# Performance work log

Measured on AMD Instinct MI355X. Metric: run time of the kernel, lower is better.

Reference implementation:

```python
import math
import jax, jax.numpy as jnp
import numpy as np

B, N = 1, 512
C_S, C_Z, H, C, P_Q, P_V = 384, 128, 12, 16, 4, 8
CAT = C_Z * H + C * H + 3 * H * P_V + 1  # 2017


def _apply(t_r, t_t, x):
    # t_r: (b,n,3,3), t_t: (b,n,3), x: (b,3,h,p,n) -> global frame coords
    xg = jnp.einsum('bnij,bjhpn->bihpn', t_r, x)
    return xg + jnp.swapaxes(t_t, 1, 2)[:, :, None, None, :]


def setup_inputs() -> dict:
    key = jax.random.key(0)
    ks = jax.random.split(key, 14)
    f = lambda k, shp: jax.random.normal(k, shp, dtype=jnp.float32)
    return {
        's': f(ks[0], (B, C_S, N)),
        'z': f(ks[1], (B, C_Z, N, N)),
        't_r': f(ks[2], (B, N, 3, 3)),
        't_t': f(ks[3], (B, N, 3)),
        'Wq': f(ks[4], (C * H, C_S)) * 0.02,
        'Wk': f(ks[5], (C * H, C_S)) * 0.02,
        'Wv': f(ks[6], (C * H, C_S)) * 0.02,
        'Wqp': f(ks[7], (3 * H * P_Q, C_S)) * 0.02,
        'Wkp': f(ks[8], (3 * H * P_Q, C_S)) * 0.02,
        'Wvp': f(ks[9], (3 * H * P_V, C_S)) * 0.02,
        'Wb': f(ks[10], (H, C_Z)) * 0.02,
        'gamma': f(ks[11], (H, 1, 1)) * 0.5,
        'Ws': f(ks[12], (C_S, CAT)) * 0.02,
        'bs': jnp.zeros((C_S,), dtype=jnp.float32),
    }


def reference(s, z, t_r, t_t, Wq, Wk, Wv, Wqp, Wkp, Wvp, Wb, gamma, Ws, bs):
    b, _, n = s.shape
    w_c = math.sqrt(2.0 / (9.0 * P_Q))
    w_l = math.sqrt(1.0 / 3.0)

    proj = lambda W: jnp.einsum('oc,bcn->bon', W, s)
    # torch rearrange 'b (c h) i -> b c h i' == reshape(b, c, h, n)
    q = proj(Wq).reshape(b, C, H, n)
    k = proj(Wk).reshape(b, C, H, n)
    v = proj(Wv).reshape(b, C, H, n)
    qp = proj(Wqp).reshape(b, 3, H, P_Q, n)
    kp = proj(Wkp).reshape(b, 3, H, P_Q, n)
    vp = proj(Wvp).reshape(b, 3, H, P_V, n)

    qg = _apply(t_r, t_t, qp)  # (b,3,h,p,n)
    kg = _apply(t_r, t_t, kp)
    diff = qg[..., :, None] - kg[..., None, :]          # (b,3,h,p,n,n)
    dist2 = jnp.sum(diff * diff, axis=(1, 3))           # sum coords + points -> (b,h,n,n)
    tmp = jax.nn.softplus(gamma)[None] * (w_c / 2.0) * dist2

    b_bias = jnp.einsum('hc,bcij->bhij', Wb, z)
    qk = jnp.einsum('bchi,bchj->bhij', q, k) / math.sqrt(C)
    a = jax.nn.softmax(w_l * (qk + b_bias - tmp), axis=-1)  # (b,h,n,n)

    o1 = jnp.einsum('bhij,bcij->bchi', a, z).reshape(b, C_Z * H, n)
    o2 = jnp.einsum('bhij,bchj->bchi', a, v).reshape(b, C * H, n)

    vg = _apply(t_r, t_t, vp)                           # (b,3,h,pv,n)
    o3g = jnp.einsum('bhij,bchpj->bchpi', a, vg)        # (b,3,h,pv,n)
    t_r_inv = jnp.swapaxes(t_r, -1, -2)
    t_t_inv = jnp.einsum('bnij,bnj->bni', -t_r_inv, t_t)
    o3 = _apply(t_r_inv, t_t_inv, o3g).reshape(b, 3 * H * P_V, n)
    o3_norm = jnp.linalg.norm(o3, axis=1, keepdims=True)  # (b,1,n)

    cat = jnp.concatenate([o1, o2, o3, o3_norm], axis=1)  # (b, CAT, n)
    return jnp.einsum('oc,bcn->bon', Ws, cat) + bs[None, :, None]
```

## Files before the change

kernel.cpp:

```cpp
#include <hip/hip_runtime.h>
#include <math.h>

#define N 512
#define H 12
#define CC 16
#define CZ 128
#define CS 384
#define PQ 4
#define PV 8
#define CATR 2017

__global__ __launch_bounds__(256) void k_proj(
    const float* __restrict__ s,
    const float* __restrict__ Wq, const float* __restrict__ Wk, const float* __restrict__ Wv,
    const float* __restrict__ Wqp, const float* __restrict__ Wkp, const float* __restrict__ Wvp,
    float* __restrict__ proj)
{
    __shared__ float Wt[16][33];
    __shared__ float St[32][128];
    int t = threadIdx.x;
    int o0 = blockIdx.x * 16;
    int n0 = blockIdx.y * 128;
    const float* Wsrc; int orow;
    if (o0 < 192)      { Wsrc = Wq;  orow = o0; }
    else if (o0 < 384) { Wsrc = Wk;  orow = o0-192; }
    else if (o0 < 576) { Wsrc = Wv;  orow = o0-384; }
    else if (o0 < 720) { Wsrc = Wqp; orow = o0-576; }
    else if (o0 < 864) { Wsrc = Wkp; orow = o0-720; }
    else               { Wsrc = Wvp; orow = o0-864; }

    int og = t >> 6, nl = t & 63;
    float acc[4][2] = {};
    for (int c0 = 0; c0 < CS; c0 += 32) {
        __syncthreads();
        for (int k = 0; k < 2; k++) {
            int idx = t + k*256;
            int oo = idx >> 5, ccol = idx & 31;
            Wt[oo][ccol] = Wsrc[(orow+oo)*CS + c0 + ccol];
        }
        for (int k = 0; k < 4; k++) {
            int idx = t + k*256;
            int ccr = idx >> 5, nn4 = idx & 31;
            float4 v = *(const float4*)&s[(c0+ccr)*N + n0 + nn4*4];
            *(float4*)&St[ccr][nn4*4] = v;
        }
        __syncthreads();
        for (int kk = 0; kk < 32; kk++) {
            float sv0 = St[kk][nl], sv1 = St[kk][nl+64];
            #pragma unroll
            for (int r = 0; r < 4; r++) {
                float w = Wt[og*4+r][kk];
                acc[r][0] += w * sv0;
                acc[r][1] += w * sv1;
            }
        }
    }
    for (int r = 0; r < 4; r++) {
        int o = o0 + og*4 + r;
        proj[o*N + n0 + nl]      = acc[r][0];
        proj[o*N + n0 + 64 + nl] = acc[r][1];
    }
}

__global__ void k_frames(const float* __restrict__ proj,
                         const float* __restrict__ t_r, const float* __restrict__ t_t,
                         float* __restrict__ qg, float* __restrict__ kg, float* __restrict__ vg)
{
    int gid = blockIdx.x * blockDim.x + threadIdx.x;
    int n = gid & (N-1);
    int hp = gid >> 9;
    if (hp >= 192) return;
    const float* src; float* dst; int rowb, stride;
    if (hp < 48)      { src = proj + 576*N; dst = qg; rowb = hp;    stride = 48; }
    else if (hp < 96) { src = proj + 720*N; dst = kg; rowb = hp-48; stride = 48; }
    else              { src = proj + 864*N; dst = vg; rowb = hp-96; stride = 96; }
    float x0 = src[(rowb + 0*stride)*N + n];
    float x1 = src[(rowb + 1*stride)*N + n];
    float x2 = src[(rowb + 2*stride)*N + n];
    #pragma unroll
    for (int d = 0; d < 3; d++) {
        float r0 = t_r[(n*3+d)*3+0], r1 = t_r[(n*3+d)*3+1], r2 = t_r[(n*3+d)*3+2];
        dst[(rowb + d*stride)*N + n] = r0*x0 + r1*x1 + r2*x2 + t_t[n*3+d];
    }
}

__global__ void k_sq(const float* __restrict__ qg, const float* __restrict__ kg,
                     float* __restrict__ sq_q, float* __restrict__ sq_k)
{
    int gid = blockIdx.x * blockDim.x + threadIdx.x;
    int n = gid & (N-1);
    int sel = gid >> 9;
    int h = sel % H;
    const float* g = (sel < H) ? qg : kg;
    float* outp = (sel < H) ? sq_q : sq_k;
    float acc = 0.f;
    #pragma unroll
    for (int d = 0; d < 3; d++)
        #pragma unroll
        for (int p = 0; p < PQ; p++) {
            float v = g[(size_t)((d*H + h)*PQ + p)*N + n];
            acc += v*v;
        }
    outp[h*N + n] = acc;
}

__global__ __launch_bounds__(256) void k_attn_o1(
    const float* __restrict__ z, const float* __restrict__ proj,
    const float* __restrict__ qg, const float* __restrict__ kg,
    const float* __restrict__ sq_q, const float* __restrict__ sq_k,
    const float* __restrict__ Wb, const float* __restrict__ gamma,
    float* __restrict__ a, float* __restrict__ cat)
{
    __shared__ float als[12*516];
    __shared__ float zls[128*68];
    int i = blockIdx.x;
    int t = threadIdx.x;
    int jl = t & 63;
    int cgu = __builtin_amdgcn_readfirstlane(t >> 6);
    const size_t NN = (size_t)N*N;
    const float w_l  = 0.57735026918962584f;
    const float w_c2 = 0.11785113019775793f;

    float ch[12];
    #pragma unroll
    for (int h = 0; h < 12; h++) {
        float g = gamma[h];
        float sp = (g > 20.f) ? g : log1pf(expf(g));
        ch[h] = sp * w_c2;
    }

    for (int jc = 0; jc < 2; jc++) {
        int j = jc*256 + jl*4;
        float acc[12][4] = {};

        {
            const float* zp = z + (size_t)(cgu*32)*NN + (size_t)i*N + j;
            for (int cc = 0; cc < 32; cc += 8) {
                float4 zb[8];
                #pragma unroll
                for (int u = 0; u < 8; u++)
                    zb[u] = *(const float4*)(zp + (size_t)(cc+u)*NN);
                #pragma unroll
                for (int u = 0; u < 8; u++) {
                    int c = cgu*32 + cc + u;
                    #pragma unroll
                    for (int h = 0; h < 12; h++) {
                        float w = Wb[h*CZ + c];
                        acc[h][0] += w*zb[u].x; acc[h][1] += w*zb[u].y;
                        acc[h][2] += w*zb[u].z; acc[h][3] += w*zb[u].w;
                    }
                }
            }
        }
        {
            const float* q  = proj;
            const float* kk = proj + 192*N;
            #pragma unroll
            for (int cc = 0; cc < 4; cc++) {
                int c = cgu*4 + cc;
                #pragma unroll
                for (int h = 0; h < 12; h++) {
                    int r = c*12 + h;
                    float qv = 0.25f * q[(size_t)r*N + i];
                    float4 k4 = *(const float4*)&kk[(size_t)r*N + j];
                    acc[h][0] += qv*k4.x; acc[h][1] += qv*k4.y;
                    acc[h][2] += qv*k4.z; acc[h][3] += qv*k4.w;
                }
            }
        }
        {
            #pragma unroll
            for (int dd = 0; dd < 3; dd++) {
                int dp = cgu*3 + dd; int d = dp >> 2, p = dp & 3;
                #pragma unroll
                for (int h = 0; h < 12; h++) {
                    int r = (d*12 + h)*4 + p;
                    float qv = 2.f * ch[h] * qg[(size_t)r*N + i];
                    float4 k4 = *(const float4*)&kg[(size_t)r*N + j];
                    acc[h][0] += qv*k4.x; acc[h][1] += qv*k4.y;
                    acc[h][2] += qv*k4.z; acc[h][3] += qv*k4.w;
                }
            }
        }

        __syncthreads();
        float* red = zls;
        if (cgu >= 2) {
            #pragma unroll
            for (int h = 0; h < 12; h++) {
                float4 v; v.x=acc[h][0]; v.y=acc[h][1]; v.z=acc[h][2]; v.w=acc[h][3];
                *(float4*)&red[(h*2 + (cgu-2))*256 + jl*4] = v;
            }
        }
        __syncthreads();
        if (cgu < 2) {
            #pragma unroll
            for (int h = 0; h < 12; h++) {
                float4 o = *(const float4*)&red[(h*2 + cgu)*256 + jl*4];
                acc[h][0] += o.x; acc[h][1] += o.y; acc[h][2] += o.z; acc[h][3] += o.w;
            }
            if (cgu == 1) {
                #pragma unroll
                for (int h = 0; h < 12; h++) {
                    float4 v; v.x=acc[h][0]; v.y=acc[h][1]; v.z=acc[h][2]; v.w=acc[h][3];
                    *(float4*)&red[(h*2 + 1)*256 + jl*4] = v;
                }
            }
        }
        __syncthreads();
        if (cgu == 0) {
            #pragma unroll
            for (int h = 0; h < 12; h++) {
                float4 o = *(const float4*)&red[(h*2 + 1)*256 + jl*4];
                float s0 = sq_q[h*N + i];
                float4 sk = *(const float4*)&sq_k[h*N + j];
                float4 r;
                r.x = w_l*(acc[h][0] + o.x - ch[h]*(s0 + sk.x));
                r.y = w_l*(acc[h][1] + o.y - ch[h]*(s0 + sk.y));
                r.z = w_l*(acc[h][2] + o.z - ch[h]*(s0 + sk.z));
                r.w = w_l*(acc[h][3] + o.w - ch[h]*(s0 + sk.w));
                *(float4*)&als[h*516 + jc*256 + jl*4] = r;
            }
        }
    }
    __syncthreads();

    #pragma unroll
    for (int hh = 0; hh < 3; hh++) {
        int h = cgu*3 + hh;
        float* row = &als[h*516 + jl*8];
        float4 v0 = *(const float4*)row;
        float4 v1 = *(const float4*)(row+4);
        float m = fmaxf(fmaxf(fmaxf(v0.x,v0.y),fmaxf(v0.z,v0.w)),
                        fmaxf(fmaxf(v1.x,v1.y),fmaxf(v1.z,v1.w)));
        for (int s = 32; s > 0; s >>= 1) m = fmaxf(m, __shfl_xor(m, s));
        v0.x = __expf(v0.x-m); v0.y = __expf(v0.y-m);
        v0.z = __expf(v0.z-m); v0.w = __expf(v0.w-m);
        v1.x = __expf(v1.x-m); v1.y = __expf(v1.y-m);
        v1.z = __expf(v1.z-m); v1.w = __expf(v1.w-m);
        float sm = v0.x+v0.y+v0.z+v0.w+v1.x+v1.y+v1.z+v1.w;
        for (int s = 32; s > 0; s >>= 1) sm += __shfl_xor(sm, s);
        float inv = 1.f/sm;
        v0.x*=inv; v0.y*=inv; v0.z*=inv; v0.w*=inv;
        v1.x*=inv; v1.y*=inv; v1.z*=inv; v1.w*=inv;
        *(float4*)row = v0;
        *(float4*)(row+4) = v1;
        float* garow = &a[((size_t)h*N + i)*N + jl*8];
        *(float4*)garow = v0;
        *(float4*)(garow+4) = v1;
    }
    __syncthreads();

    int cg = t & 31, hg = (t>>5)&1, jq = t>>6;
    float acc[4][6] = {};
    for (int jc = 0; jc < 8; jc++) {
        __syncthreads();
        #pragma unroll
        for (int k = 0; k < 8; k++) {
            int idx = t + k*256;
            int c = idx >> 4, j4 = idx & 15;
            *(float4*)&zls[c*68 + j4*4] =
                *(const float4*)&z[((size_t)c*N + i)*N + jc*64 + j4*4];
        }
        __syncthreads();
        #pragma unroll
        for (int s = 0; s < 4; s++) {
            int jo = jq*16 + s*4;
            float4 a4[6];
            #pragma unroll
            for (int hh = 0; hh < 6; hh++)
                a4[hh] = *(const float4*)&als[(hg*6+hh)*516 + jc*64 + jo];
            #pragma unroll
            for (int r = 0; r < 4; r++) {
                float4 zz = *(const float4*)&zls[(cg + 32*r)*68 + jo];
                #pragma unroll
                for (int hh = 0; hh < 6; hh++)
                    acc[r][hh] += zz.x*a4[hh].x + zz.y*a4[hh].y
                                + zz.z*a4[hh].z + zz.w*a4[hh].w;
            }
        }
    }
    __syncthreads();
    if (jq >= 2) {
        float* rb = &zls[((jq-2)*128 + (t & 127))*25];
        #pragma unroll
        for (int r = 0; r < 4; r++)
            #pragma unroll
            for (int hh = 0; hh < 6; hh++) rb[r*6+hh] = acc[r][hh];
    }
    __syncthreads();
    if (jq < 2) {
        const float* rb = &zls[(jq*128 + (t & 127))*25];
        #pragma unroll
        for (int r = 0; r < 4; r++)
            #pragma unroll
            for (int hh = 0; hh < 6; hh++) acc[r][hh] += rb[r*6+hh];
        if (jq == 1) {
            float* rb2 = &als[(t & 63)*25];
            #pragma unroll
            for (int r = 0; r < 4; r++)
                #pragma unroll
                for (int hh = 0; hh < 6; hh++) rb2[r*6+hh] = acc[r][hh];
        }
    }
    __syncthreads();
    if (jq == 0) {
        const float* rb2 = &als[t*25];
        #pragma unroll
        for (int r = 0; r < 4; r++)
            #pragma unroll
            for (int hh = 0; hh < 6; hh++) {
                float v = acc[r][hh] + rb2[r*6+hh];
                int c = cg + 32*r;
                int h = hg*6 + hh;
                cat[(size_t)(c*H + h)*N + i] = v;
            }
    }
}

__global__ __launch_bounds__(256) void k_o2o3g(
    const float* __restrict__ a, const float* __restrict__ proj, const float* __restrict__ vg,
    float* __restrict__ cat, float* __restrict__ o3g)
{
    __shared__ float ats[8*132];
    __shared__ float vts[40*132];
    int h = blockIdx.x, i0 = blockIdx.y*8;
    int t = threadIdx.x;
    int il = t & 7, rg = (t>>3)&7, jq = t>>6;
    const float* v = proj + 384*N;
    float acc[5] = {};
    for (int jc = 0; jc < 4; jc++) {
        __syncthreads();
        {
            int ii = t >> 5, j4 = t & 31;
            *(float4*)&ats[ii*132 + j4*4] =
                *(const float4*)&a[((size_t)h*N + i0+ii)*N + jc*128 + j4*4];
        }
        #pragma unroll
        for (int k = 0; k < 5; k++) {
            int idx = t + k*256;
            int r = idx >> 5, j4 = idx & 31;
            const float* src = (r < 16) ? (v + (size_t)(r*H + h)*N)
                : (vg + (size_t)(((r-16)>>3)*96 + h*PV + ((r-16)&7))*N);
            *(float4*)&vts[r*132 + j4*4] = *(const float4*)&src[jc*128 + j4*4];
        }
        __syncthreads();
        #pragma unroll
        for (int s = 0; s < 8; s++) {
            int jo = jq*32 + s*4;
            float4 a4 = *(const float4*)&ats[il*132 + jo];
            #pragma unroll
            for (int r = 0; r < 5; r++) {
                float4 v4 = *(const float4*)&vts[(rg*5+r)*132 + jo];
                acc[r] += v4.x*a4.x + v4.y*a4.y + v4.z*a4.z + v4.w*a4.w;
            }
        }
    }
    __syncthreads();
    if (jq >= 2) {
        float* rb = &ats[((jq-2)*64 + (t & 63))*5];
        #pragma unroll
        for (int r = 0; r < 5; r++) rb[r] = acc[r];
    }
    __syncthreads();
    if (jq < 2) {
        const float* rb = &ats[(jq*64 + (t & 63))*5];
        #pragma unroll
        for (int r = 0; r < 5; r++) acc[r] += rb[r];
        if (jq == 1) {
            float* rb2 = &ats[640 + (t & 63)*5];
            #pragma unroll
            for (int r = 0; r < 5; r++) rb2[r] = acc[r];
        }
    }
    __syncthreads();
    if (jq == 0) {
        const float* rb2 = &ats[640 + t*5];
        #pragma unroll
        for (int r = 0; r < 5; r++) {
            float val = acc[r] + rb2[r];
            int row = rg*5 + r;
            if (row < 16) cat[(size_t)(1536 + row*H + h)*N + i0 + il] = val;
            else { int rr = row - 16;
                   o3g[(size_t)((rr>>3)*96 + h*PV + (rr&7))*N + i0 + il] = val; }
        }
    }
}

__global__ void k_o3(const float* __restrict__ o3g,
                     const float* __restrict__ t_r, const float* __restrict__ t_t,
                     float* __restrict__ cat)
{
    int gid = blockIdx.x*blockDim.x + threadIdx.x;
    int i = gid & (N-1), hp = gid >> 9;
    if (hp >= 96) return;
    float x0 = o3g[(size_t)(0*96 + hp)*N + i] - t_t[i*3+0];
    float x1 = o3g[(size_t)(1*96 + hp)*N + i] - t_t[i*3+1];
    float x2 = o3g[(size_t)(2*96 + hp)*N + i] - t_t[i*3+2];
    #pragma unroll
    for (int d = 0; d < 3; d++) {
        float o = t_r[(i*3+0)*3+d]*x0 + t_r[(i*3+1)*3+d]*x1 + t_r[(i*3+2)*3+d]*x2;
        cat[(size_t)(1728 + d*96 + hp)*N + i] = o;
    }
}

__global__ void k_norm(float* __restrict__ cat)
{
    int i = blockIdx.x*blockDim.x + threadIdx.x;
    if (i >= N) return;
    float acc = 0.f;
    for (int r = 0; r < 288; r++) {
        float v = cat[(size_t)(1728+r)*N + i];
        acc += v*v;
    }
    cat[(size_t)2016*N + i] = sqrtf(acc);
}

__global__ __launch_bounds__(256) void k_final(
    const float* __restrict__ Ws, const float* __restrict__ bs,
    const float* __restrict__ cat, float* __restrict__ out)
{
    __shared__ float Wt[16*33];
    __shared__ float Ct[32*66];
    int o0 = blockIdx.x*16, n0 = blockIdx.y*64;
    int ks = blockIdx.z;
    int kbeg = ks*505, kend = min(CATR, kbeg+505);
    int t = threadIdx.x;
    int og = t >> 6, nl = t & 63;
    float acc[4] = {};
    for (int c0 = kbeg; c0 < kend; c0 += 32) {
        __syncthreads();
        for (int k = 0; k < 2; k++) {
            int idx = t + k*256;
            int oo = idx >> 5, ccol = idx & 31;
            int c = c0 + ccol;
            Wt[oo*33 + ccol] = (c < kend) ? Ws[(size_t)(o0+oo)*CATR + c] : 0.f;
        }
        for (int k = 0; k < 4; k++) {
            int idx = t + k*256;
            int ccr = idx >> 5, j2 = idx & 31;
            int c = c0 + ccr;
            float2 vv; vv.x = 0.f; vv.y = 0.f;
            if (c < kend) vv = *(const float2*)&cat[(size_t)c*N + n0 + j2*2];
            *(float2*)&Ct[ccr*66 + j2*2] = vv;
        }
        __syncthreads();
        int klim = min(32, kend - c0);
        for (int kk = 0; kk < klim; kk++) {
            float cv = Ct[kk*66 + nl];
            #pragma unroll
            for (int r = 0; r < 4; r++)
                acc[r] += Wt[(og*4+r)*33 + kk] * cv;
        }
    }
    #pragma unroll
    for (int r = 0; r < 4; r++) {
        int o = o0 + og*4 + r;
        float val = acc[r];
        if (ks == 0) val += bs[o];
        atomicAdd(&out[(size_t)o*N + n0 + nl], val);
    }
}

extern "C" void kernel_launch(void* const* d_in, const int* in_sizes, int n_in,
                              void* d_out, int out_size, void* d_ws, size_t ws_size,
                              hipStream_t stream)
{
    const float* s     = (const float*)d_in[0];
    const float* z     = (const float*)d_in[1];
    const float* t_r   = (const float*)d_in[2];
    const float* t_t   = (const float*)d_in[3];
    const float* Wq    = (const float*)d_in[4];
    const float* Wk    = (const float*)d_in[5];
    const float* Wv    = (const float*)d_in[6];
    const float* Wqp   = (const float*)d_in[7];
    const float* Wkp   = (const float*)d_in[8];
    const float* Wvp   = (const float*)d_in[9];
    const float* Wb    = (const float*)d_in[10];
    const float* gamma = (const float*)d_in[11];
    const float* Ws    = (const float*)d_in[12];
    const float* bs    = (const float*)d_in[13];
    float* out = (float*)d_out;

    float* ws   = (float*)d_ws;
    float* proj = ws;
    float* qg   = proj + 1152*N;
    float* kg   = qg   + 144*N;
    float* vg   = kg   + 144*N;
    float* sq_q = vg   + 288*N;
    float* sq_k = sq_q + H*N;
    float* o3g  = sq_k + H*N;
    float* a    = o3g  + 288*N;
    float* cat  = a    + (size_t)H*N*N;

    k_proj   <<<dim3(72,4),   256, 0, stream>>>(s, Wq, Wk, Wv, Wqp, Wkp, Wvp, proj);
    k_frames <<<384,          256, 0, stream>>>(proj, t_r, t_t, qg, kg, vg);
    k_sq     <<<48,           256, 0, stream>>>(qg, kg, sq_q, sq_k);
    k_attn_o1<<<512,          256, 0, stream>>>(z, proj, qg, kg, sq_q, sq_k, Wb, gamma, a, cat);
    k_o2o3g  <<<dim3(12,64),  256, 0, stream>>>(a, proj, vg, cat, o3g);
    k_o3     <<<192,          256, 0, stream>>>(o3g, t_r, t_t, cat);
    k_norm   <<<2,            256, 0, stream>>>(cat);
    hipMemsetAsync(out, 0, (size_t)CS*N*sizeof(float), stream);
    k_final  <<<dim3(24,8,4), 256, 0, stream>>>(Ws, bs, cat, out);
}
```

Before: 409.0 us.

## Split fused attention kernel into logits/softmax and j-split o1 kernels with atomics

Splits the fused attention+o1 kernel into two. The first computes logits and softmax for one row with 512 threads, one j per thread, and folds the squared-norm kernel into it. The second computes the o1 contraction over a 4-way j-split grid, accumulating into a zero-initialised cat through atomicAdd. The norm kernel is also parallelised over more blocks. The aim is more parallelism and occupancy, at the cost of reading z twice from memory, an extra write and read of a, and atomics.

```diff
diff --git a/kernel.cpp b/kernel.cpp
--- a/kernel.cpp
+++ b/kernel.cpp
@@ -84,236 +84,184 @@
     }
 }
 
-__global__ void k_sq(const float* __restrict__ qg, const float* __restrict__ kg,
-                     float* __restrict__ sq_q, float* __restrict__ sq_k)
-{
-    int gid = blockIdx.x * blockDim.x + threadIdx.x;
-    int n = gid & (N-1);
-    int sel = gid >> 9;
-    int h = sel % H;
-    const float* g = (sel < H) ? qg : kg;
-    float* outp = (sel < H) ? sq_q : sq_k;
-    float acc = 0.f;
-    #pragma unroll
-    for (int d = 0; d < 3; d++)
-        #pragma unroll
-        for (int p = 0; p < PQ; p++) {
-            float v = g[(size_t)((d*H + h)*PQ + p)*N + n];
-            acc += v*v;
-        }
-    outp[h*N + n] = acc;
-}
-
-__global__ __launch_bounds__(256) void k_attn_o1(
+__global__ __launch_bounds__(512, 4) void k_logits(
     const float* __restrict__ z, const float* __restrict__ proj,
     const float* __restrict__ qg, const float* __restrict__ kg,
-    const float* __restrict__ sq_q, const float* __restrict__ sq_k,
     const float* __restrict__ Wb, const float* __restrict__ gamma,
-    float* __restrict__ a, float* __restrict__ cat)
-{
-    __shared__ float als[12*516];
-    __shared__ float zls[128*68];
-    int i = blockIdx.x;
-    int t = threadIdx.x;
-    int jl = t & 63;
-    int cgu = __builtin_amdgcn_readfirstlane(t >> 6);
-    const size_t NN = (size_t)N*N;
+    float* __restrict__ a)
+{
+    __shared__ float pm[12][8];
+    __shared__ float ps[12][8];
+    const int i = blockIdx.x;
+    const int t = threadIdx.x;
+    const int w = t >> 6;
+    const int l = t & 63;
+    const size_t NN = (size_t)N * N;
     const float w_l  = 0.57735026918962584f;
     const float w_c2 = 0.11785113019775793f;
 
     float ch[12];
     #pragma unroll
-    for (int h = 0; h < 12; h++) {
+    for (int h = 0; h < 12; ++h) {
         float g = gamma[h];
         float sp = (g > 20.f) ? g : log1pf(expf(g));
         ch[h] = sp * w_c2;
     }
 
-    for (int jc = 0; jc < 2; jc++) {
-        int j = jc*256 + jl*4;
-        float acc[12][4] = {};
-
-        {
-            const float* zp = z + (size_t)(cgu*32)*NN + (size_t)i*N + j;
-            for (int cc = 0; cc < 32; cc += 8) {
-                float4 zb[8];
+    float acc[12] = {};
+
+    {
+        const float* zp = z + (size_t)i*N + t;
+        for (int c0 = 0; c0 < CZ; c0 += 8) {
+            float zb[8];
+            #pragma unroll
+            for (int u = 0; u < 8; ++u) zb[u] = zp[(size_t)(c0+u)*NN];
+            #pragma unroll
+            for (int h = 0; h < 12; ++h)
                 #pragma unroll
-                for (int u = 0; u < 8; u++)
-                    zb[u] = *(const float4*)(zp + (size_t)(cc+u)*NN);
+                for (int u = 0; u < 8; ++u)
+                    acc[h] = fmaf(Wb[h*CZ + c0 + u], zb[u], acc[h]);
+        }
+    }
+    {
+        const float* qq = proj;
+        const float* kk = proj + 192*N;
+        for (int c = 0; c < 16; ++c) {
+            float kv[12];
+            #pragma unroll
+            for (int h = 0; h < 12; ++h)
+                kv[h] = kk[(size_t)(c*12+h)*N + t];
+            #pragma unroll
+            for (int h = 0; h < 12; ++h)
+                acc[h] = fmaf(0.25f * qq[(size_t)(c*12+h)*N + i], kv[h], acc[h]);
+        }
+    }
+    float k2[12] = {}, q2[12] = {};
+    for (int dp = 0; dp < 12; ++dp) {
+        int d = dp >> 2, p = dp & 3;
+        #pragma unroll
+        for (int h = 0; h < 12; ++h) {
+            int r = (d*12 + h)*4 + p;
+            float kv = kg[(size_t)r*N + t];
+            float qv = qg[(size_t)r*N + i];
+            acc[h] = fmaf(2.f*ch[h]*qv, kv, acc[h]);
+            k2[h]  = fmaf(kv, kv, k2[h]);
+            q2[h]  = fmaf(qv, qv, q2[h]);
+        }
+    }
+
+    float lv[12], mw[12];
+    #pragma unroll
+    for (int h = 0; h < 12; ++h)
+        lv[h] = w_l * (acc[h] - ch[h]*(q2[h] + k2[h]));
+
+    #pragma unroll
+    for (int h = 0; h < 12; ++h) {
+        float m = lv[h];
+        for (int s = 32; s; s >>= 1) m = fmaxf(m, __shfl_xor(m, s));
+        float e = __expf(lv[h] - m);
+        float sm = e;
+        for (int s = 32; s; s >>= 1) sm += __shfl_xor(sm, s);
+        lv[h] = e; mw[h] = m;
+        if (l == 0) { pm[h][w] = m; ps[h][w] = sm; }
+    }
+    __syncthreads();
+    #pragma unroll
+    for (int h = 0; h < 12; ++h) {
+        float mg = pm[h][0];
+        #pragma unroll
+        for (int u = 1; u < 8; ++u) mg = fmaxf(mg, pm[h][u]);
+        float sg = 0.f;
+        #pragma unroll
+        for (int u = 0; u < 8; ++u) sg += ps[h][u] * __expf(pm[h][u] - mg);
+        float f = __expf(mw[h] - mg) / sg;
+        a[((size_t)h*N + i)*N + t] = lv[h] * f;
+    }
+}
+
+__global__ __launch_bounds__(256, 4) void k_o1(
+    const float* __restrict__ a, const float* __restrict__ z,
+    float* __restrict__ cat)
+{
+    __shared__ float als[12][132];
+    __shared__ float zls[128*36];
+    const int i  = blockIdx.x;
+    const int j0 = blockIdx.y * 128;
+    const int t  = threadIdx.x;
+
+    #pragma unroll
+    for (int k = 0; k < 2; ++k) {
+        int id = t + k*256;
+        if (id < 384) {
+            int h = id >> 5, j4 = id & 31;
+            *(float4*)&als[h][j4*4] =
+                *(const float4*)&a[((size_t)h*N + i)*N + j0 + j4*4];
+        }
+    }
+    const int cg = t & 31, hg = (t >> 5) & 1, jq = t >> 6;
+    float acc[4][6] = {};
+    for (int jc = 0; jc < 4; ++jc) {
+        __syncthreads();
+        #pragma unroll
+        for (int k = 0; k < 4; ++k) {
+            int idx = t + k*256;
+            int c = idx >> 3, j4 = idx & 7;
+            *(float4*)&zls[c*36 + j4*4] =
+                *(const float4*)&z[((size_t)c*N + i)*N + j0 + jc*32 + j4*4];
+        }
+        __syncthreads();
+        #pragma unroll
+        for (int s = 0; s < 2; ++s) {
+            int jo = jq*8 + s*4;
+            float4 a4[6];
+            #pragma unroll
+            for (int hh = 0; hh < 6; ++hh)
+                a4[hh] = *(const float4*)&als[hg*6+hh][jc*32 + jo];
+            #pragma unroll
+            for (int r = 0; r < 4; ++r) {
+                float4 z4 = *(const float4*)&zls[(cg + 32*r)*36 + jo];
                 #pragma unroll
-                for (int u = 0; u < 8; u++) {
-                    int c = cgu*32 + cc + u;
-                    #pragma unroll
-                    for (int h = 0; h < 12; h++) {
-                        float w = Wb[h*CZ + c];
-                        acc[h][0] += w*zb[u].x; acc[h][1] += w*zb[u].y;
-                        acc[h][2] += w*zb[u].z; acc[h][3] += w*zb[u].w;
-                    }
-                }
+                for (int hh = 0; hh < 6; ++hh)
+                    acc[r][hh] += z4.x*a4[hh].x + z4.y*a4[hh].y
+                                + z4.z*a4[hh].z + z4.w*a4[hh].w;
             }
         }
-        {
-            const float* q  = proj;
-            const float* kk = proj + 192*N;
-            #pragma unroll
-            for (int cc = 0; cc < 4; cc++) {
-                int c = cgu*4 + cc;
-                #pragma unroll
-                for (int h = 0; h < 12; h++) {
-                    int r = c*12 + h;
-                    float qv = 0.25f * q[(size_t)r*N + i];
-                    float4 k4 = *(const float4*)&kk[(size_t)r*N + j];
-                    acc[h][0] += qv*k4.x; acc[h][1] += qv*k4.y;
-                    acc[h][2] += qv*k4.z; acc[h][3] += qv*k4.w;
-                }
-            }
-        }
-        {
-            #pragma unroll
-            for (int dd = 0; dd < 3; dd++) {
-                int dp = cgu*3 + dd; int d = dp >> 2, p = dp & 3;
-                #pragma unroll
-                for (int h = 0; h < 12; h++) {
-                    int r = (d*12 + h)*4 + p;
-                    float qv = 2.f * ch[h] * qg[(size_t)r*N + i];
-                    float4 k4 = *(const float4*)&kg[(size_t)r*N + j];
-                    acc[h][0] += qv*k4.x; acc[h][1] += qv*k4.y;
-                    acc[h][2] += qv*k4.z; acc[h][3] += qv*k4.w;
-                }
-            }
-        }
-
-        __syncthreads();
-        float* red = zls;
-        if (cgu >= 2) {
-            #pragma unroll
-            for (int h = 0; h < 12; h++) {
-                float4 v; v.x=acc[h][0]; v.y=acc[h][1]; v.z=acc[h][2]; v.w=acc[h][3];
-                *(float4*)&red[(h*2 + (cgu-2))*256 + jl*4] = v;
-            }
-        }
-        __syncthreads();
-        if (cgu < 2) {
-            #pragma unroll
-            for (int h = 0; h < 12; h++) {
-                float4 o = *(const float4*)&red[(h*2 + cgu)*256 + jl*4];
-                acc[h][0] += o.x; acc[h][1] += o.y; acc[h][2] += o.z; acc[h][3] += o.w;
-            }
-            if (cgu == 1) {
-                #pragma unroll
-                for (int h = 0; h < 12; h++) {
-                    float4 v; v.x=acc[h][0]; v.y=acc[h][1]; v.z=acc[h][2]; v.w=acc[h][3];
-                    *(float4*)&red[(h*2 + 1)*256 + jl*4] = v;
-                }
-            }
-        }
-        __syncthreads();
-        if (cgu == 0) {
-            #pragma unroll
-            for (int h = 0; h < 12; h++) {
-                float4 o = *(const float4*)&red[(h*2 + 1)*256 + jl*4];
-                float s0 = sq_q[h*N + i];
-                float4 sk = *(const float4*)&sq_k[h*N + j];
-                float4 r;
-                r.x = w_l*(acc[h][0] + o.x - ch[h]*(s0 + sk.x));
-                r.y = w_l*(acc[h][1] + o.y - ch[h]*(s0 + sk.y));
-                r.z = w_l*(acc[h][2] + o.z - ch[h]*(s0 + sk.z));
-                r.w = w_l*(acc[h][3] + o.w - ch[h]*(s0 + sk.w));
-                *(float4*)&als[h*516 + jc*256 + jl*4] = r;
-            }
-        }
-    }
-    __syncthreads();
-
-    #pragma unroll
-    for (int hh = 0; hh < 3; hh++) {
-        int h = cgu*3 + hh;
-        float* row = &als[h*516 + jl*8];
-        float4 v0 = *(const float4*)row;
-        float4 v1 = *(const float4*)(row+4);
-        float m = fmaxf(fmaxf(fmaxf(v0.x,v0.y),fmaxf(v0.z,v0.w)),
-                        fmaxf(fmaxf(v1.x,v1.y),fmaxf(v1.z,v1.w)));
-        for (int s = 32; s > 0; s >>= 1) m = fmaxf(m, __shfl_xor(m, s));
-        v0.x = __expf(v0.x-m); v0.y = __expf(v0.y-m);
-        v0.z = __expf(v0.z-m); v0.w = __expf(v0.w-m);
-        v1.x = __expf(v1.x-m); v1.y = __expf(v1.y-m);
-        v1.z = __expf(v1.z-m); v1.w = __expf(v1.w-m);
-        float sm = v0.x+v0.y+v0.z+v0.w+v1.x+v1.y+v1.z+v1.w;
-        for (int s = 32; s > 0; s >>= 1) sm += __shfl_xor(sm, s);
-        float inv = 1.f/sm;
-        v0.x*=inv; v0.y*=inv; v0.z*=inv; v0.w*=inv;
-        v1.x*=inv; v1.y*=inv; v1.z*=inv; v1.w*=inv;
-        *(float4*)row = v0;
-        *(float4*)(row+4) = v1;
-        float* garow = &a[((size_t)h*N + i)*N + jl*8];
-        *(float4*)garow = v0;
-        *(float4*)(garow+4) = v1;
-    }
-    __syncthreads();
-
-    int cg = t & 31, hg = (t>>5)&1, jq = t>>6;
-    float acc[4][6] = {};
-    for (int jc = 0; jc < 8; jc++) {
-        __syncthreads();
-        #pragma unroll
-        for (int k = 0; k < 8; k++) {
-            int idx = t + k*256;
-            int c = idx >> 4, j4 = idx & 15;
-            *(float4*)&zls[c*68 + j4*4] =
-                *(const float4*)&z[((size_t)c*N + i)*N + jc*64 + j4*4];
-        }
-        __syncthreads();
-        #pragma unroll
-        for (int s = 0; s < 4; s++) {
-            int jo = jq*16 + s*4;
-            float4 a4[6];
-            #pragma unroll
-            for (int hh = 0; hh < 6; hh++)
-                a4[hh] = *(const float4*)&als[(hg*6+hh)*516 + jc*64 + jo];
-            #pragma unroll
-            for (int r = 0; r < 4; r++) {
-                float4 zz = *(const float4*)&zls[(cg + 32*r)*68 + jo];
-                #pragma unroll
-                for (int hh = 0; hh < 6; hh++)
-                    acc[r][hh] += zz.x*a4[hh].x + zz.y*a4[hh].y
-                                + zz.z*a4[hh].z + zz.w*a4[hh].w;
-            }
-        }
-    }
+    }
+    const int sl = t & 63;
     __syncthreads();
     if (jq >= 2) {
-        float* rb = &zls[((jq-2)*128 + (t & 127))*25];
-        #pragma unroll
-        for (int r = 0; r < 4; r++)
-            #pragma unroll
-            for (int hh = 0; hh < 6; hh++) rb[r*6+hh] = acc[r][hh];
+        float* rb = &zls[(jq-2)*1600 + sl*25];
+        #pragma unroll
+        for (int r = 0; r < 4; ++r)
+            #pragma unroll
+            for (int hh = 0; hh < 6; ++hh) rb[r*6+hh] = acc[r][hh];
     }
     __syncthreads();
     if (jq < 2) {
-        const float* rb = &zls[(jq*128 + (t & 127))*25];
-        #pragma unroll
-        for (int r = 0; r < 4; r++)
-            #pragma unroll
-            for (int hh = 0; hh < 6; hh++) acc[r][hh] += rb[r*6+hh];
-        if (jq == 1) {
-            float* rb2 = &als[(t & 63)*25];
-            #pragma unroll
-            for (int r = 0; r < 4; r++)
-                #pragma unroll
-                for (int hh = 0; hh < 6; hh++) rb2[r*6+hh] = acc[r][hh];
-        }
+        const float* rb = &zls[jq*1600 + sl*25];
+        #pragma unroll
+        for (int r = 0; r < 4; ++r)
+            #pragma unroll
+            for (int hh = 0; hh < 6; ++hh) acc[r][hh] += rb[r*6+hh];
+    }
+    __syncthreads();
+    if (jq == 1) {
+        float* rb = &zls[sl*25];
+        #pragma unroll
+        for (int r = 0; r < 4; ++r)
+            #pragma unroll
+            for (int hh = 0; hh < 6; ++hh) rb[r*6+hh] = acc[r][hh];
     }
     __syncthreads();
     if (jq == 0) {
-        const float* rb2 = &als[t*25];
-        #pragma unroll
-        for (int r = 0; r < 4; r++)
-            #pragma unroll
-            for (int hh = 0; hh < 6; hh++) {
-                float v = acc[r][hh] + rb2[r*6+hh];
-                int c = cg + 32*r;
-                int h = hg*6 + hh;
-                cat[(size_t)(c*H + h)*N + i] = v;
+        const float* rb = &zls[sl*25];
+        #pragma unroll
+        for (int r = 0; r < 4; ++r)
+            #pragma unroll
+            for (int hh = 0; hh < 6; ++hh) {
+                float v = acc[r][hh] + rb[r*6+hh];
+                int c = cg + 32*r, h = hg*6 + hh;
+                atomicAdd(&cat[(size_t)(c*H + h)*N + i], v);
             }
     }
 }
@@ -406,14 +354,22 @@
 
 __global__ void k_norm(float* __restrict__ cat)
 {
-    int i = blockIdx.x*blockDim.x + threadIdx.x;
-    if (i >= N) return;
+    __shared__ float red[8][32];
+    int il = threadIdx.x & 31, g = threadIdx.x >> 5;
+    int i = blockIdx.x*32 + il;
     float acc = 0.f;
-    for (int r = 0; r < 288; r++) {
+    for (int r = g*36; r < g*36 + 36; ++r) {
         float v = cat[(size_t)(1728+r)*N + i];
         acc += v*v;
     }
-    cat[(size_t)2016*N + i] = sqrtf(acc);
+    red[g][il] = acc;
+    __syncthreads();
+    if (g == 0) {
+        acc = 0.f;
+        #pragma unroll
+        for (int u = 0; u < 8; ++u) acc += red[u][il];
+        cat[(size_t)2016*N + i] = sqrtf(acc);
+    }
 }
 
 __global__ __launch_bounds__(256) void k_final(
@@ -487,19 +443,19 @@
     float* qg   = proj + 1152*N;
     float* kg   = qg   + 144*N;
     float* vg   = kg   + 144*N;
-    float* sq_q = vg   + 288*N;
-    float* sq_k = sq_q + H*N;
-    float* o3g  = sq_k + H*N;
+    float* o3g  = vg   + 288*N;
     float* a    = o3g  + 288*N;
     float* cat  = a    + (size_t)H*N*N;
 
+    hipMemsetAsync(cat, 0, (size_t)1536*N*sizeof(float), stream);
+
     k_proj   <<<dim3(72,4),   256, 0, stream>>>(s, Wq, Wk, Wv, Wqp, Wkp, Wvp, proj);
     k_frames <<<384,          256, 0, stream>>>(proj, t_r, t_t, qg, kg, vg);
-    k_sq     <<<48,           256, 0, stream>>>(qg, kg, sq_q, sq_k);
-    k_attn_o1<<<512,          256, 0, stream>>>(z, proj, qg, kg, sq_q, sq_k, Wb, gamma, a, cat);
+    k_logits <<<512,          512, 0, stream>>>(z, proj, qg, kg, Wb, gamma, a);
+    k_o1     <<<dim3(512,4),  256, 0, stream>>>(a, z, cat);
     k_o2o3g  <<<dim3(12,64),  256, 0, stream>>>(a, proj, vg, cat, o3g);
     k_o3     <<<192,          256, 0, stream>>>(o3g, t_r, t_t, cat);
-    k_norm   <<<2,            256, 0, stream>>>(cat);
+    k_norm   <<<16,           256, 0, stream>>>(cat);
     hipMemsetAsync(out, 0, (size_t)CS*N*sizeof(float), stream);
     k_final  <<<dim3(24,8,4), 256, 0, stream>>>(Ws, bs, cat, out);
 }
```

New measurement: 631.6 us. +54.4%, slower.
